# Kernel optimization log

Hardware: AMD Instinct MI355X
Metric: run time of the kernel (lower is better)

Reference implementation:

```python
import jax, jax.numpy as jnp
import numpy as np

N_NODES = 50000


def setup_inputs() -> dict:
    key = jax.random.key(0)
    k1, k2, k3, k4 = jax.random.split(key, 4)
    N, E, D_IN, D_OUT = N_NODES, 1_600_000, 128, 128
    x = jax.random.normal(k1, (N, D_IN), dtype=jnp.float32)
    edge_index = jax.random.randint(k2, (2, E), 0, N, dtype=jnp.int64)
    W = jax.random.normal(k3, (D_IN, D_OUT), dtype=jnp.float32) * (1.0 / np.sqrt(D_IN))
    b = jax.random.normal(k4, (D_OUT,), dtype=jnp.float32) * 0.01
    return {"x": x, "edge_index": edge_index, "W": W, "b": b}


def reference(x, edge_index, W, b):
    N = x.shape[0]
    # add self loops: edge (i, i) for every node
    loops = jnp.arange(N, dtype=edge_index.dtype)
    row = jnp.concatenate([edge_index[0], loops])  # [E+N]
    col = jnp.concatenate([edge_index[1], loops])  # [E+N]
    # degree over col (matches torch_geometric degree(col, N))
    deg = jax.ops.segment_sum(jnp.ones_like(col, dtype=x.dtype), col, num_segments=N)
    deg_inv_sqrt = jnp.where(deg > 0, jax.lax.rsqrt(jnp.maximum(deg, 1.0)), 0.0)
    norm = deg_inv_sqrt[row] * deg_inv_sqrt[col]  # [E+N]
    # linear transform then gather-multiply-scatter (segment sum over row)
    xl = x @ W + b  # [N, D_OUT]
    msg = norm[:, None] * xl[col]  # [E+N, D_OUT]
    out = jax.ops.segment_sum(msg, row, num_segments=N)
    return out
```

## Files before the change

kernel.cpp:

```cpp
#include <hip/hip_runtime.h>
#include <hip/hip_bf16.h>


#define D     128
#define TILE  8192
#define BINB  1024
#define RPB   256
#define MAXB  256
#define SPLIT_CAP 16384
#define DSEG  4
#define DTIL  32

typedef short  bf16x8 __attribute__((ext_vector_type(8)));
typedef float  f32x4  __attribute__((ext_vector_type(4)));
typedef unsigned short us4 __attribute__((ext_vector_type(4)));
typedef unsigned short us8 __attribute__((ext_vector_type(8)));

static __device__ __forceinline__ unsigned short f2bf(float f) {
    unsigned u = __float_as_uint(f);
    u = (u + 0x7FFFu + ((u >> 16) & 1u)) >> 16;
    return (unsigned short)u;
}
static __device__ __forceinline__ float bf2f(unsigned short s) {
    return __uint_as_float(((unsigned)s) << 16);
}

__global__ __launch_bounds__(256) void k_init(int* __restrict__ cntc,
                                              int* __restrict__ bcur,
                                              int N, int NB, int CAP) {
    int i = blockIdx.x * 256 + threadIdx.x;
    if (i < N) cntc[i] = 0;
    if (i < NB) bcur[i] = i * CAP;
}

__global__ __launch_bounds__(256) void k_prepw(const float* __restrict__ W,
                                               unsigned short* __restrict__ wtb) {
    int g = blockIdx.x * 256 + threadIdx.x;
    int n = g >> 7, k = g & 127;
    wtb[n * 128 + k] = f2bf(W[k * 128 + n]);
}

__global__ __launch_bounds__(BINB) void k_bin(const int* __restrict__ rows,
                                              const int* __restrict__ cols,
                                              int* __restrict__ bcur,
                                              unsigned* __restrict__ ebuf,
                                              int E, int NB, int CAP) {
    __shared__ int lcnt[MAXB];
    __shared__ int lbase[MAXB];
    const int t = threadIdx.x;
    const int base = blockIdx.x * TILE;
    int m = E - base; if (m > TILE) m = TILE;

    unsigned p[TILE / BINB];
    #pragma unroll
    for (int it = 0; it < TILE / BINB; ++it) {
        int i = it * BINB + t;
        if (i < m) {
            unsigned r = (unsigned)rows[base + i];
            unsigned c = (unsigned)cols[base + i];
            p[it] = c | ((r & 255u) << 16) | ((r >> 8) << 24);
        }
    }
    for (int b = t; b < NB; b += BINB) lcnt[b] = 0;
    __syncthreads();
    #pragma unroll
    for (int it = 0; it < TILE / BINB; ++it) {
        int i = it * BINB + t;
        if (i < m) atomicAdd(&lcnt[p[it] >> 24], 1);
    }
    __syncthreads();
    for (int b = t; b < NB; b += BINB) {
        int c = lcnt[b];
        lbase[b] = c ? atomicAdd(&bcur[b], c) : 0;
        lcnt[b] = 0;
    }
    __syncthreads();
    #pragma unroll
    for (int it = 0; it < TILE / BINB; ++it) {
        int i = it * BINB + t;
        if (i < m) {
            int bk = p[it] >> 24;
            int r  = atomicAdd(&lcnt[bk], 1);
            int pos = lbase[bk] + r;
            if (pos < (bk + 1) * CAP)
                ebuf[pos] = p[it] & 0xFFFFFFu;
        }
    }
}

__global__ __launch_bounds__(1024) void k_deg2(const int* __restrict__ cols,
                                               int* __restrict__ cntc,
                                               int E, int N) {
    const int segw = (N + DSEG - 1) / DSEG;
    __shared__ int h[12544];
    const int seg  = blockIdx.x & (DSEG - 1);
    const int tile = blockIdx.x >> 2;
    const int lo = seg * segw;
    const int hi = min(lo + segw, N);
    const int w  = hi - lo;
    for (int i = threadIdx.x; i < w; i += 1024) h[i] = 0;
    __syncthreads();
    const int per = (E + DTIL - 1) / DTIL;
    const int beg = tile * per;
    const int end = min(beg + per, E);
    for (int i = beg + threadIdx.x; i < end; i += 1024) {
        int c = cols[i];
        if (c >= lo && c < hi) atomicAdd(&h[c - lo], 1);
    }
    __syncthreads();
    for (int i = threadIdx.x; i < w; i += 1024) {
        int v = h[i];
        if (v) atomicAdd(&cntc[lo + i], v);
    }
}

__global__ __launch_bounds__(256) void k_dis(const int* __restrict__ cntc,
                                             float* __restrict__ dis, int N) {
    int i = blockIdx.x * 256 + threadIdx.x;
    if (i < N) dis[i] = rsqrtf((float)(cntc[i] + 1));
}

__global__ __launch_bounds__(1024) void k_split(const int* __restrict__ bcur,
                                                const unsigned* __restrict__ ebuf,
                                                unsigned short* __restrict__ ecol,
                                                int* __restrict__ begN,
                                                int* __restrict__ endN,
                                                int N, int CAP) {
    __shared__ unsigned short sorted[SPLIT_CAP];
    __shared__ int cnt[RPB];
    __shared__ int excl[RPB];
    __shared__ int cur[RPB];
    const int b = blockIdx.x, t = threadIdx.x;
    const int base = b * CAP;
    int m = bcur[b] - base; if (m > CAP) m = CAP;
    if (t < RPB) cnt[t] = 0;
    __syncthreads();
    for (int i = t; i < m; i += 1024)
        atomicAdd(&cnt[(ebuf[base + i] >> 16) & 255], 1);
    __syncthreads();
    if (t == 0) {
        int s = 0;
        #pragma unroll
        for (int r = 0; r < RPB; ++r) { excl[r] = s; s += cnt[r]; }
    }
    __syncthreads();
    const int row0 = b * RPB;
    if (t < RPB) {
        cur[t] = excl[t];
        if (row0 + t < N) {
            begN[row0 + t] = base + excl[t];
            endN[row0 + t] = base + excl[t] + cnt[t];
        }
    }
    __syncthreads();
    for (int i = t; i < m; i += 1024) {
        unsigned p = ebuf[base + i];
        int pos = atomicAdd(&cur[(p >> 16) & 255], 1);
        sorted[pos] = (unsigned short)(p & 0xFFFFu);
    }
    __syncthreads();
    for (int i = t; i < m; i += 1024)
        ecol[base + i] = sorted[i];
}

__global__ __launch_bounds__(256) void k_gemm(const float* __restrict__ x,
                                              const unsigned short* __restrict__ wtb,
                                              const float* __restrict__ bia,
                                              unsigned short* __restrict__ xlb,
                                              int N) {
    __shared__ unsigned short wt[128][136];
    __shared__ unsigned short xs[64][136];
    const int t = threadIdx.x;
    const int row0 = blockIdx.x * 64;

    #pragma unroll
    for (int i = 0; i < 8; ++i) {
        int j = i * 256 + t;
        int n = j >> 4, k8 = j & 15;
        us8 v = *(const us8*)&wtb[j * 8];
        *(us8*)&wt[n][k8 * 8] = v;
    }
    #pragma unroll
    for (int i = 0; i < 8; ++i) {
        int j = i * 256 + t;
        int r = j >> 5, c4 = j & 31;
        int gr = row0 + r;
        us4 o = (us4){0, 0, 0, 0};
        if (gr < N) {
            float4 v = *(const float4*)&x[(size_t)gr * D + c4 * 4];
            o = (us4){f2bf(v.x), f2bf(v.y), f2bf(v.z), f2bf(v.w)};
        }
        *(us4*)&xs[r][c4 * 4] = o;
    }
    __syncthreads();

    const int w  = t >> 6, l = t & 63;
    const int m0 = w * 16;
    const int lm = l & 15, lq = l >> 4;

    f32x4 acc[8];
    #pragma unroll
    for (int nt = 0; nt < 8; ++nt) acc[nt] = (f32x4){0.f, 0.f, 0.f, 0.f};

    #pragma unroll
    for (int kk = 0; kk < 4; ++kk) {
        const int kof = kk * 32 + lq * 8;
        bf16x8 a = *(const bf16x8*)&xs[m0 + lm][kof];
        #pragma unroll
        for (int nt = 0; nt < 8; ++nt) {
            bf16x8 bb = *(const bf16x8*)&wt[nt * 16 + lm][kof];
            acc[nt] = __builtin_amdgcn_mfma_f32_16x16x32_bf16(a, bb, acc[nt], 0, 0, 0);
        }
    }

    #pragma unroll
    for (int nt = 0; nt < 8; ++nt) {
        const int col = nt * 16 + lm;
        const float bc = bia[col];
        #pragma unroll
        for (int r = 0; r < 4; ++r) {
            int grow = row0 + m0 + lq * 4 + r;
            if (grow < N) xlb[(size_t)grow * D + col] = f2bf(acc[nt][r] + bc);
        }
    }
}

__global__ __launch_bounds__(256) void k_reduce(const int* __restrict__ begN,
                                                const int* __restrict__ endN,
                                                const unsigned short* __restrict__ ecol,
                                                const float* __restrict__ dis,
                                                const unsigned short* __restrict__ xlb,
                                                float* __restrict__ out, int N) {
    const int wave = threadIdx.x >> 6;
    const int lane = threadIdx.x & 63;
    const int i = blockIdx.x * 4 + wave;
    if (i >= N) return;
    const float di = dis[i];

    const ushort2 sv = *reinterpret_cast<const ushort2*>(xlb + (size_t)i * D + lane * 2);
    float ax = di * di * bf2f(sv.x);
    float ay = di * di * bf2f(sv.y);

    const int beg = begN[i], end = endN[i];
    for (int base = beg; base < end; base += 64) {
        int m = end - base; if (m > 64) m = 64;
        int   c = 0;
        float n = 0.0f;
        if (lane < m) {
            c = ecol[base + lane];
            n = di * dis[c];
        }
        for (int j = 0; j < m; j += 8) {
            float vx[8], vy[8], nn[8];
            #pragma unroll
            for (int u = 0; u < 8; ++u) {
                int cc = __shfl(c, j + u);
                ushort2 s = *reinterpret_cast<const ushort2*>(xlb + (size_t)cc * D + lane * 2);
                vx[u] = bf2f(s.x);
                vy[u] = bf2f(s.y);
                nn[u] = __shfl(n, j + u);
            }
            #pragma unroll
            for (int u = 0; u < 8; ++u) {
                ax = fmaf(nn[u], vx[u], ax);
                ay = fmaf(nn[u], vy[u], ay);
            }
        }
    }
    *reinterpret_cast<float2*>(out + (size_t)i * D + lane * 2) = make_float2(ax, ay);
}

__global__ __launch_bounds__(256) void k_zero(int* __restrict__ p, int n) {
    int i = blockIdx.x * 256 + threadIdx.x;
    if (i < n) p[i] = 0;
}
__global__ __launch_bounds__(256) void k_deg(const int* __restrict__ cols,
                                             int* __restrict__ cntc, int E) {
    int e = blockIdx.x * 256 + threadIdx.x;
    if (e < E) atomicAdd(&cntc[cols[e]], 1);
}
#define GEMM_R 8
__global__ __launch_bounds__(128) void k_gemmf(const float* __restrict__ x,
                                               const float* __restrict__ W,
                                               const float* __restrict__ b,
                                               float* __restrict__ xl, int N) {
    __shared__ float xs[GEMM_R][D];
    const int c  = threadIdx.x;
    const int r0 = blockIdx.x * GEMM_R;
    #pragma unroll
    for (int r = 0; r < GEMM_R; ++r) {
        int row = r0 + r;
        xs[r][c] = (row < N) ? x[row * D + c] : 0.0f;
    }
    __syncthreads();
    float acc[GEMM_R];
    const float bc = b[c];
    #pragma unroll
    for (int r = 0; r < GEMM_R; ++r) acc[r] = bc;
    for (int k = 0; k < D; k += 4) {
        const float w0 = W[(k + 0) * D + c];
        const float w1 = W[(k + 1) * D + c];
        const float w2 = W[(k + 2) * D + c];
        const float w3 = W[(k + 3) * D + c];
        #pragma unroll
        for (int r = 0; r < GEMM_R; ++r) {
            const float4 xv = *reinterpret_cast<const float4*>(&xs[r][k]);
            acc[r] = fmaf(xv.x, w0, acc[r]);
            acc[r] = fmaf(xv.y, w1, acc[r]);
            acc[r] = fmaf(xv.z, w2, acc[r]);
            acc[r] = fmaf(xv.w, w3, acc[r]);
        }
    }
    #pragma unroll
    for (int r = 0; r < GEMM_R; ++r) {
        int row = r0 + r;
        if (row < N) xl[row * D + c] = acc[r];
    }
}
__global__ __launch_bounds__(256) void k_self(const float* __restrict__ xl,
                                              const float* __restrict__ dis,
                                              float* __restrict__ out, int N) {
    int gid = blockIdx.x * 256 + threadIdx.x;
    int i = gid >> 7;
    if (i < N) {
        float d = dis[i];
        out[gid] = d * d * xl[gid];
    }
}
__global__ __launch_bounds__(256) void k_scatter(const int* __restrict__ rows,
                                                 const int* __restrict__ cols,
                                                 const float* __restrict__ dis,
                                                 const float* __restrict__ xl,
                                                 float* __restrict__ out, int E) {
    long long gid = (long long)blockIdx.x * 256 + threadIdx.x;
    int e    = (int)(gid >> 6);
    int lane = (int)(gid & 63);
    if (e >= E) return;
    const int row = rows[e];
    const int col = cols[e];
    const float nrm = dis[row] * dis[col];
    atomicAdd(&out[row * D + lane],      nrm * xl[col * D + lane]);
    atomicAdd(&out[row * D + 64 + lane], nrm * xl[col * D + 64 + lane]);
}

extern "C" void kernel_launch(void* const* d_in, const int* in_sizes, int n_in,
                              void* d_out, int out_size, void* d_ws, size_t ws_size,
                              hipStream_t stream) {
    const float* x   = (const float*)d_in[0];
    const int*   ei  = (const int*)d_in[1];
    const float* W   = (const float*)d_in[2];
    const float* b   = (const float*)d_in[3];
    float*       out = (float*)d_out;

    const int N = in_sizes[0] / D;
    const int E = in_sizes[1] / 2;
    const int* rows = ei;
    const int* cols = ei + E;
    const int NB = (N + RPB - 1) / RPB;
    const int NT = (E + TILE - 1) / TILE;
    const int CAP = (((2 * E) / NB) + 63) / 64 * 64;

    char* p = (char*)d_ws;
    size_t off = 0;
    unsigned short* xlb  = (unsigned short*)(p + off); off += (size_t)N * D * 2;
    unsigned short* wtb  = (unsigned short*)(p + off); off += (size_t)D * D * 2;
    float*          dis  = (float*)(p + off);          off += (size_t)N * 4;
    int*            cntc = (int*)(p + off);            off += (size_t)N * 4;
    int*            bcur = (int*)(p + off);            off += (size_t)MAXB * 4;
    int*            begN = (int*)(p + off);            off += (size_t)N * 4;
    int*            endN = (int*)(p + off);            off += (size_t)N * 4;
    unsigned*       ebuf = (unsigned*)(p + off);       off += (size_t)NB * CAP * 4;
    unsigned short* ecol = (unsigned short*)(p + off); off += (size_t)NB * CAP * 2;

    const int gN = (N + 255) / 256;
    const int gE = (E + 255) / 256;

    if (N <= 65536 && NB <= MAXB && CAP <= SPLIT_CAP && ws_size >= off) {
        k_init  <<<gN, 256, 0, stream>>>(cntc, bcur, N, NB, CAP);
        k_prepw <<<(D * D) / 256, 256, 0, stream>>>(W, wtb);
        k_bin   <<<NT, BINB, 0, stream>>>(rows, cols, bcur, ebuf, E, NB, CAP);
        k_deg2  <<<DTIL * DSEG, 1024, 0, stream>>>(cols, cntc, E, N);
        k_dis   <<<gN, 256, 0, stream>>>(cntc, dis, N);
        k_split <<<NB, 1024, 0, stream>>>(bcur, ebuf, ecol, begN, endN, N, CAP);
        k_gemm  <<<(N + 63) / 64, 256, 0, stream>>>(x, wtb, b, xlb, N);
        k_reduce<<<(N + 3) / 4, 256, 0, stream>>>(begN, endN, ecol, dis, xlb, out, N);
    } else {
        char* q = (char*)d_ws;
        float* xl   = (float*)q;
        float* disF = (float*)(q + (size_t)N * D * 4);
        int*   cc   = (int*)(q + (size_t)N * D * 4 + (size_t)N * 4);
        k_zero <<<gN, 256, 0, stream>>>(cc, N);
        k_deg  <<<gE, 256, 0, stream>>>(cols, cc, E);
        k_dis  <<<gN, 256, 0, stream>>>(cc, disF, N);
        k_gemmf<<<(N + GEMM_R - 1) / GEMM_R, 128, 0, stream>>>(x, W, b, xl, N);
        k_self <<<((N * D) + 255) / 256, 256, 0, stream>>>(xl, disF, out, N);
        long long st = (long long)E * 64;
        k_scatter<<<(int)((st + 255) / 256), 256, 0, stream>>>(rows, cols, disF, xl, out, E);
    }
}
```

Before: 197.4 us.

## Sort edges by column segment within rows and widen reduce gathers

The split kernel now buckets each row's edges by a coarse column segment (16 segments) using a parallel prefix scan instead of a serial one. Within a row the gathered xl rows are then ordered by column, which is meant to improve cache locality. The reduce kernel splits each wave into two half-waves that each gather 8-byte chunks for different edges, then combines the halves with shuffles. The W-prep and init kernels are merged into one launch to save a launch.

After: 200.1 us. No clear change (+1.4%).

```diff
diff --git a/kernel.cpp b/kernel.cpp
--- a/kernel.cpp
+++ b/kernel.cpp
@@ -8,6 +8,7 @@
 #define RPB   256
 #define MAXB  256
 #define SPLIT_CAP 16384
+#define CSEG  16
 #define DSEG  4
 #define DTIL  32
 
@@ -25,19 +26,18 @@
     return __uint_as_float(((unsigned)s) << 16);
 }
 
-__global__ __launch_bounds__(256) void k_init(int* __restrict__ cntc,
+__global__ __launch_bounds__(256) void k_prep(const float* __restrict__ W,
+                                              unsigned short* __restrict__ wtb,
+                                              int* __restrict__ cntc,
                                               int* __restrict__ bcur,
                                               int N, int NB, int CAP) {
     int i = blockIdx.x * 256 + threadIdx.x;
     if (i < N) cntc[i] = 0;
     if (i < NB) bcur[i] = i * CAP;
-}
-
-__global__ __launch_bounds__(256) void k_prepw(const float* __restrict__ W,
-                                               unsigned short* __restrict__ wtb) {
-    int g = blockIdx.x * 256 + threadIdx.x;
-    int n = g >> 7, k = g & 127;
-    wtb[n * 128 + k] = f2bf(W[k * 128 + n]);
+    if (i < D * D) {
+        int n = i >> 7, k = i & 127;
+        wtb[n * 128 + k] = f2bf(W[k * 128 + n]);
+    }
 }
 
 __global__ __launch_bounds__(BINB) void k_bin(const int* __restrict__ rows,
@@ -125,37 +125,48 @@
                                                 unsigned short* __restrict__ ecol,
                                                 int* __restrict__ begN,
                                                 int* __restrict__ endN,
-                                                int N, int CAP) {
+                                                int N, int CAP, int colshift) {
     __shared__ unsigned short sorted[SPLIT_CAP];
-    __shared__ int cnt[RPB];
-    __shared__ int excl[RPB];
-    __shared__ int cur[RPB];
+    __shared__ int cnt[RPB * CSEG];
+    __shared__ int psum[1024];
     const int b = blockIdx.x, t = threadIdx.x;
     const int base = b * CAP;
     int m = bcur[b] - base; if (m > CAP) m = CAP;
-    if (t < RPB) cnt[t] = 0;
-    __syncthreads();
-    for (int i = t; i < m; i += 1024)
-        atomicAdd(&cnt[(ebuf[base + i] >> 16) & 255], 1);
-    __syncthreads();
-    if (t == 0) {
-        int s = 0;
-        #pragma unroll
-        for (int r = 0; r < RPB; ++r) { excl[r] = s; s += cnt[r]; }
-    }
-    __syncthreads();
-    const int row0 = b * RPB;
-    if (t < RPB) {
-        cur[t] = excl[t];
-        if (row0 + t < N) {
-            begN[row0 + t] = base + excl[t];
-            endN[row0 + t] = base + excl[t] + cnt[t];
-        }
-    }
+    #pragma unroll
+    for (int u = 0; u < 4; ++u) cnt[u * 1024 + t] = 0;
     __syncthreads();
     for (int i = t; i < m; i += 1024) {
         unsigned p = ebuf[base + i];
-        int pos = atomicAdd(&cur[(p >> 16) & 255], 1);
+        int key = (int)((p >> 16) & 255) * CSEG + (int)((p & 0xFFFFu) >> colshift);
+        atomicAdd(&cnt[key], 1);
+    }
+    __syncthreads();
+    int a0 = cnt[4 * t], a1 = cnt[4 * t + 1], a2 = cnt[4 * t + 2], a3 = cnt[4 * t + 3];
+    int tot = a0 + a1 + a2 + a3;
+    psum[t] = tot;
+    __syncthreads();
+    for (int off = 1; off < 1024; off <<= 1) {
+        int add = (t >= off) ? psum[t - off] : 0;
+        __syncthreads();
+        psum[t] += add;
+        __syncthreads();
+    }
+    int ex = psum[t] - tot;
+    cnt[4 * t]     = ex;
+    cnt[4 * t + 1] = ex + a0;
+    cnt[4 * t + 2] = ex + a0 + a1;
+    cnt[4 * t + 3] = ex + a0 + a1 + a2;
+    __syncthreads();
+    const int row0 = b * RPB;
+    if (t < RPB && row0 + t < N) {
+        begN[row0 + t] = base + cnt[t * CSEG];
+        endN[row0 + t] = base + ((t == RPB - 1) ? m : cnt[(t + 1) * CSEG]);
+    }
+    __syncthreads();
+    for (int i = t; i < m; i += 1024) {
+        unsigned p = ebuf[base + i];
+        int key = (int)((p >> 16) & 255) * CSEG + (int)((p & 0xFFFFu) >> colshift);
+        int pos = atomicAdd(&cnt[key], 1);
         sorted[pos] = (unsigned short)(p & 0xFFFFu);
     }
     __syncthreads();
@@ -233,41 +244,56 @@
                                                 float* __restrict__ out, int N) {
     const int wave = threadIdx.x >> 6;
     const int lane = threadIdx.x & 63;
+    const int half = lane >> 5;
+    const int hl   = lane & 31;
     const int i = blockIdx.x * 4 + wave;
     if (i >= N) return;
     const float di = dis[i];
 
-    const ushort2 sv = *reinterpret_cast<const ushort2*>(xlb + (size_t)i * D + lane * 2);
-    float ax = di * di * bf2f(sv.x);
-    float ay = di * di * bf2f(sv.y);
+    float a0 = 0.f, a1 = 0.f, a2 = 0.f, a3 = 0.f;
+    if (half == 0) {
+        uint2 s = *(const uint2*)(xlb + (size_t)i * D + hl * 4);
+        float w = di * di;
+        a0 = w * __uint_as_float(s.x << 16);
+        a1 = w * __uint_as_float(s.x & 0xFFFF0000u);
+        a2 = w * __uint_as_float(s.y << 16);
+        a3 = w * __uint_as_float(s.y & 0xFFFF0000u);
+    }
 
     const int beg = begN[i], end = endN[i];
     for (int base = beg; base < end; base += 64) {
         int m = end - base; if (m > 64) m = 64;
-        int   c = 0;
-        float n = 0.0f;
+        int c = 0; float n = 0.f;
         if (lane < m) {
             c = ecol[base + lane];
             n = di * dis[c];
         }
-        for (int j = 0; j < m; j += 8) {
-            float vx[8], vy[8], nn[8];
+        for (int j = 0; j < m; j += 16) {
+            uint2 dv[8]; float nn[8];
             #pragma unroll
             for (int u = 0; u < 8; ++u) {
-                int cc = __shfl(c, j + u);
-                ushort2 s = *reinterpret_cast<const ushort2*>(xlb + (size_t)cc * D + lane * 2);
-                vx[u] = bf2f(s.x);
-                vy[u] = bf2f(s.y);
-                nn[u] = __shfl(n, j + u);
+                int slot = j + 2 * u + half;
+                int cc = __shfl(c, slot);
+                nn[u] = __shfl(n, slot);
+                dv[u] = *(const uint2*)(xlb + (size_t)cc * D + hl * 4);
             }
             #pragma unroll
             for (int u = 0; u < 8; ++u) {
-                ax = fmaf(nn[u], vx[u], ax);
-                ay = fmaf(nn[u], vy[u], ay);
+                a0 = fmaf(nn[u], __uint_as_float(dv[u].x << 16),         a0);
+                a1 = fmaf(nn[u], __uint_as_float(dv[u].x & 0xFFFF0000u), a1);
+                a2 = fmaf(nn[u], __uint_as_float(dv[u].y << 16),         a2);
+                a3 = fmaf(nn[u], __uint_as_float(dv[u].y & 0xFFFF0000u), a3);
             }
         }
     }
-    *reinterpret_cast<float2*>(out + (size_t)i * D + lane * 2) = make_float2(ax, ay);
+    float b0 = __shfl(a0, hl + 32);
+    float b1 = __shfl(a1, hl + 32);
+    float b2 = __shfl(a2, hl + 32);
+    float b3 = __shfl(a3, hl + 32);
+    if (half == 0) {
+        float4 o = make_float4(a0 + b0, a1 + b1, a2 + b2, a3 + b3);
+        *(float4*)(out + (size_t)i * D + hl * 4) = o;
+    }
 }
 
 __global__ __launch_bounds__(256) void k_zero(int* __restrict__ p, int n) {
@@ -360,6 +386,9 @@
     const int NT = (E + TILE - 1) / TILE;
     const int CAP = (((2 * E) / NB) + 63) / 64 * 64;
 
+    int colshift = 0;
+    while (((N - 1) >> colshift) >= CSEG) ++colshift;
+
     char* p = (char*)d_ws;
     size_t off = 0;
     unsigned short* xlb  = (unsigned short*)(p + off); off += (size_t)N * D * 2;
@@ -376,12 +405,11 @@
     const int gE = (E + 255) / 256;
 
     if (N <= 65536 && NB <= MAXB && CAP <= SPLIT_CAP && ws_size >= off) {
-        k_init  <<<gN, 256, 0, stream>>>(cntc, bcur, N, NB, CAP);
-        k_prepw <<<(D * D) / 256, 256, 0, stream>>>(W, wtb);
+        k_prep  <<<gN, 256, 0, stream>>>(W, wtb, cntc, bcur, N, NB, CAP);
         k_bin   <<<NT, BINB, 0, stream>>>(rows, cols, bcur, ebuf, E, NB, CAP);
         k_deg2  <<<DTIL * DSEG, 1024, 0, stream>>>(cols, cntc, E, N);
         k_dis   <<<gN, 256, 0, stream>>>(cntc, dis, N);
-        k_split <<<NB, 1024, 0, stream>>>(bcur, ebuf, ecol, begN, endN, N, CAP);
+        k_split <<<NB, 1024, 0, stream>>>(bcur, ebuf, ecol, begN, endN, N, CAP, colshift);
         k_gemm  <<<(N + 63) / 64, 256, 0, stream>>>(x, wtb, b, xlb, N);
         k_reduce<<<(N + 3) / 4, 256, 0, stream>>>(begN, endN, ecol, dis, xlb, out, N);
     } else {
```
